# Kernel tuning notes

Measured on AMD Instinct MI355X. Metric: run time of the kernel, lower is better.

The kernel has to match this reference:

```python
import jax, jax.numpy as jnp
import numpy as np

HID, INP, BATCH, TIME = 1024, 512, 128, 256


def _kaiming(key, d1, d2, gain):
    # kaiming_normal_: std = gain / sqrt(fan_in), fan_in = d2
    return jax.random.normal(key, (d1, d2), jnp.float32) * (gain / np.sqrt(d2))


def setup_inputs() -> dict:
    key = jax.random.key(0)
    ks = jax.random.split(key, 9)
    g_lin = 1.0          # nonlinearity='linear'
    g_tanh = 5.0 / 3.0   # nonlinearity='tanh'
    inp = {
        "x": jax.random.normal(ks[0], (BATCH, TIME, INP), jnp.float32),
        "c": jnp.zeros((HID, BATCH), jnp.float32),
        "h": jnp.zeros((HID, BATCH), jnp.float32),
        "W_gx": _kaiming(ks[1], HID, INP, g_lin),
        "W_ix": _kaiming(ks[2], HID, INP, g_lin),
        "W_fx": _kaiming(ks[3], HID, INP, g_lin),
        "W_ox": _kaiming(ks[4], HID, INP, g_lin),
        "W_gh": _kaiming(ks[5], HID, HID, g_tanh),
        "W_ih": _kaiming(ks[6], HID, HID, g_tanh),
        "W_fh": _kaiming(ks[7], HID, HID, g_tanh),
        "W_oh": _kaiming(ks[8], HID, HID, g_tanh),
        "b_g": jnp.zeros((HID, 1), jnp.float32),
        "b_i": jnp.zeros((HID, 1), jnp.float32),
        "b_f": jnp.zeros((HID, 1), jnp.float32),
        "b_o": jnp.zeros((HID, 1), jnp.float32),
    }
    return inp


def reference(x, c, h, W_gx, W_ix, W_fx, W_ox, W_gh, W_ih, W_fh, W_oh,
              b_g, b_i, b_f, b_o):
    Hd = W_gx.shape[0]
    # Fuse the four gate GEMMs into one: same math, single contraction.
    Wx = jnp.concatenate([W_gx, W_ix, W_fx, W_ox], axis=0)   # (4H, I)
    Wh = jnp.concatenate([W_gh, W_ih, W_fh, W_oh], axis=0)   # (4H, H)
    b = jnp.concatenate([b_g, b_i, b_f, b_o], axis=0)[:, 0]  # (4H,)
    # Precompute all input projections: (T, B, 4H)
    xs = jnp.einsum('bti,gi->tbg', x, Wx)

    def step(carry, xt):
        c_t, h_t = carry                      # (B, H)
        z = xt + h_t @ Wh.T + b               # (B, 4H)
        g = jnp.tanh(z[:, :Hd])
        i = jax.nn.sigmoid(z[:, Hd:2 * Hd])
        f = jax.nn.sigmoid(z[:, 2 * Hd:3 * Hd])
        o = jax.nn.sigmoid(z[:, 3 * Hd:])
        c_n = g * i + c_t * f
        h_n = jnp.tanh(c_n) * o
        return (c_n, h_n), None

    (c_f, h_f), _ = jax.lax.scan(step, (c.T, h.T), xs)
    return h_f.T  # (H, B), matching the torch layout
```

## Files before the change

### kernel.cpp

```cpp
#include <hip/hip_runtime.h>
#include <cstdint>
#include <cstddef>

#define HID 1024
#define INP 512
#define BATCH 128
#define TSTEPS 256
#define NK16 96
#define HSLOTS 32
#define NBLK_CHUNK 256
#define HSLOT ((size_t)64 * 4 * 2 * 512)

using short8  = __attribute__((ext_vector_type(8))) short;
using f32x16  = __attribute__((ext_vector_type(16))) float;

#define LD8(p) (*(const short8*)(p))
#define MFMA32(a,b,c) __builtin_amdgcn_mfma_f32_32x32x16_bf16((a),(b),(c),0,0,0)

static __device__ __forceinline__ unsigned short f2bf(float f) {
    union { float f; unsigned int u; } v; v.f = f;
    unsigned int r = v.u + 0x7fffu + ((v.u >> 16) & 1u);
    return (unsigned short)(r >> 16);
}
static __device__ __forceinline__ float bf2f(unsigned short b) {
    union { unsigned int u; float f; } v; v.u = ((unsigned int)b) << 16;
    return v.f;
}
static __device__ __forceinline__ float sigmoid_f(float z) {
    return 1.0f / (1.0f + __expf(-z));
}
static __device__ __forceinline__ float tanh_f(float z) {
    return 2.0f / (1.0f + __expf(-2.0f * z)) - 1.0f;
}


__global__ void prep_w(const float* __restrict__ Wgx, const float* __restrict__ Wix,
                       const float* __restrict__ Wfx, const float* __restrict__ Wox,
                       const float* __restrict__ Wgh, const float* __restrict__ Wih,
                       const float* __restrict__ Wfh, const float* __restrict__ Woh,
                       unsigned short* __restrict__ wfrag)
{
    const int k16 = blockIdx.x;
    const int s   = blockIdx.y;
    const int tid  = threadIdx.x;
    const int lane = tid >> 2;
    const int e0   = (tid & 3) * 2;
    const int row  = s * 32 + (lane & 31);
    const int k    = k16 * 16 + (lane >> 5) * 8 + e0;
    const int j = row >> 2;
    const int g = row & 3;
    float f0, f1;
    if (k < INP) {
        const float* wx = (g == 0 ? Wgx : g == 1 ? Wix : g == 2 ? Wfx : Wox) + (size_t)j * INP;
        f0 = wx[k]; f1 = wx[k + 1];
    } else {
        const float* wh = (g == 0 ? Wgh : g == 1 ? Wih : g == 2 ? Wfh : Woh) + (size_t)j * HID;
        f0 = wh[k - INP]; f1 = wh[k - INP + 1];
    }
    ushort2 hi, lo;
    hi.x = f2bf(f0); lo.x = f2bf(f0 - bf2f(hi.x));
    hi.y = f2bf(f1); lo.y = f2bf(f1 - bf2f(hi.y));
    unsigned short* base = wfrag + ((size_t)(s * NK16 + k16) * 2) * 512 + lane * 8 + e0;
    *(ushort2*)(base)       = hi;
    *(ushort2*)(base + 512) = lo;
}

__global__ void prep_x(const float* __restrict__ x, unsigned short* __restrict__ xfrag)
{
    const int k16x = blockIdx.x;
    const int t    = blockIdx.y;
    const int tid  = threadIdx.x;
    const int cg   = tid >> 6;
    const int lane = tid & 63;
    const int col  = cg * 32 + (lane & 31);
    const int k0   = k16x * 16 + (lane >> 5) * 8;
    const float* src = x + ((size_t)col * TSTEPS + t) * INP + k0;
    const float4 v0 = *(const float4*)(src);
    const float4 v1 = *(const float4*)(src + 4);
    ushort4 h0, l0, h1, l1;
    h0.x = f2bf(v0.x); l0.x = f2bf(v0.x - bf2f(h0.x));
    h0.y = f2bf(v0.y); l0.y = f2bf(v0.y - bf2f(h0.y));
    h0.z = f2bf(v0.z); l0.z = f2bf(v0.z - bf2f(h0.z));
    h0.w = f2bf(v0.w); l0.w = f2bf(v0.w - bf2f(h0.w));
    h1.x = f2bf(v1.x); l1.x = f2bf(v1.x - bf2f(h1.x));
    h1.y = f2bf(v1.y); l1.y = f2bf(v1.y - bf2f(h1.y));
    h1.z = f2bf(v1.z); l1.z = f2bf(v1.z - bf2f(h1.z));
    h1.w = f2bf(v1.w); l1.w = f2bf(v1.w - bf2f(h1.w));
    unsigned short* base = xfrag +
        ((size_t)(((size_t)t * 32 + k16x) * 4 + cg) * 2) * 512 + lane * 8;
    *(ushort4*)(base)           = h0;
    *(ushort4*)(base + 4)       = h1;
    *(ushort4*)(base + 512)     = l0;
    *(ushort4*)(base + 512 + 4) = l1;
}

__global__ void prep_state(const float* __restrict__ cin, const float* __restrict__ hin,
                           float* __restrict__ cdst, unsigned short* __restrict__ hslot,
                           unsigned* __restrict__ flags)
{
    if (blockIdx.x == 0) flags[threadIdx.x] = 0u;
    const int idx = blockIdx.x * 256 + threadIdx.x;
    cdst[idx] = cin[idx];
    const int j = idx >> 7;
    const int b = idx & 127;
    float f = hin[idx];
    unsigned short hh = f2bf(f);
    unsigned short hl = f2bf(f - bf2f(hh));
    const int k16h = j >> 4;
    const int hlf  = (j >> 3) & 1;
    const int e    = j & 7;
    const int cg   = b >> 5;
    const int lane = 32 * hlf + (b & 31);
    unsigned short* base = hslot +
        ((size_t)((k16h * 4 + cg) * 2) * 512) + lane * 8 + e;
    base[0]   = hh;
    base[512] = hl;
}

__global__ __launch_bounds__(512, 1) void lstm_persist(
    const unsigned short* __restrict__ wfrag,
    const unsigned short* __restrict__ xfrag,
    unsigned short* __restrict__ hbuf,
    float* __restrict__ cst,
    const float* __restrict__ bg, const float* __restrict__ bi,
    const float* __restrict__ bf_, const float* __restrict__ bo,
    float* __restrict__ outf,
    unsigned* __restrict__ flags)
{
    const int tid  = threadIdx.x;
    const int wv   = tid >> 6;
    const int lane = tid & 63;
    const int l31  = lane & 31;
    const int hl   = lane >> 5;
    const int bx   = blockIdx.x;

    const int xcd     = bx & 7;
    const int ii      = bx >> 3;
    const int s       = xcd * 16 + (ii >> 1);
    const int cb      = ii & 1;
    const int colbase = cb << 6;

    const int ejl  = tid >> 6;
    const int ecl  = tid & 63;
    const int ej   = s * 8 + ejl;
    const int ecol = colbase + ecl;
    const size_t ci = (size_t)ej * BATCH + ecol;

    const float bias0 = bg[ej], bias1 = bi[ej], bias2 = bf_[ej], bias3 = bo[ej];
    float creg = cst[ci];

    const size_t bOff = (size_t)(4 * wv + 2 * cb) * 1024 + lane * 8;
    const int k16h = s >> 1;

    const unsigned short* pAx0 = wfrag + ((size_t)(s * NK16 + wv) * 2) * 512 + lane * 8;
    const unsigned short* pAh0 = wfrag + ((size_t)(s * NK16 + 32 + wv) * 2) * 512 + lane * 8;

    __shared__ float part[8][32][64];
    __shared__ unsigned long long hstage[256];
    unsigned short* hs16 = (unsigned short*)hstage;

#pragma unroll 1
    for (int t = 0; t < TSTEPS; ++t) {
        f32x16 a0A, a0B, a1A, a1B;
#pragma unroll
        for (int r = 0; r < 16; ++r) { a0A[r]=0.f; a0B[r]=0.f; a1A[r]=0.f; a1B[r]=0.f; }

        {
            const unsigned short* pA = pAx0;
            const unsigned short* pX = xfrag + (size_t)t * 131072 + bOff;
#pragma unroll
            for (int m = 0; m < 4; ++m) {
                short8 Ah  = LD8(pA);
                short8 Al  = LD8(pA + 512);
                short8 B0h = LD8(pX);
                short8 B0l = LD8(pX + 512);
                short8 B1h = LD8(pX + 1024);
                short8 B1l = LD8(pX + 1536);
                pA += 8192; pX += 32768;
                a0A = MFMA32(Ah, B0h, a0A);
                a1A = MFMA32(Ah, B1h, a1A);
                a0B = MFMA32(Ah, B0l, a0B);
                a1B = MFMA32(Ah, B1l, a1B);
                a0A = MFMA32(Al, B0h, a0A);
                a1A = MFMA32(Al, B1h, a1A);
            }
        }

        if (t > 0) {
            const unsigned target = (unsigned)t;
            int done;
            int guard = 0;
            do {
                unsigned v = target;
                if (tid < 256)
                    v = __hip_atomic_load(&flags[tid], __ATOMIC_RELAXED,
                                          __HIP_MEMORY_SCOPE_AGENT);
                done = __syncthreads_count(v >= target);
                if (done < 512) __builtin_amdgcn_s_sleep(1);
            } while (done < 512 && ++guard < (1 << 20));
            asm volatile("" ::: "memory");
            __builtin_amdgcn_sched_barrier(0);
            if ((t & 31) == 0)
                __builtin_amdgcn_fence(__ATOMIC_ACQUIRE, "agent");
        }

        {
            const unsigned short* pA = pAh0;
            const unsigned short* pH = hbuf + (size_t)((t + HSLOTS - 1) & (HSLOTS - 1)) * HSLOT + bOff;
#pragma unroll
            for (int m = 0; m < 8; ++m) {
                short8 Ah  = LD8(pA);
                short8 Al  = LD8(pA + 512);
                short8 B0h = LD8(pH);
                short8 B0l = LD8(pH + 512);
                short8 B1h = LD8(pH + 1024);
                short8 B1l = LD8(pH + 1536);
                pA += 8192; pH += 32768;
                a0A = MFMA32(Ah, B0h, a0A);
                a1A = MFMA32(Ah, B1h, a1A);
                a0B = MFMA32(Ah, B0l, a0B);
                a1B = MFMA32(Ah, B1l, a1B);
                a0A = MFMA32(Al, B0h, a0A);
                a1A = MFMA32(Al, B1h, a1A);
            }
        }

#pragma unroll
        for (int r = 0; r < 16; ++r) {
            const int lr = (r & 3) + 8 * (r >> 2) + 4 * hl;
            part[wv][lr][l31]      = a0A[r] + a0B[r];
            part[wv][lr][32 + l31] = a1A[r] + a1B[r];
        }
        __syncthreads();

        {
            const int r0 = 4 * ejl;
            float z0g = bias0, z1g = bias1, z2g = bias2, z3g = bias3;
#pragma unroll
            for (int p = 0; p < 8; ++p) {
                z0g += part[p][r0 + 0][ecl];
                z1g += part[p][r0 + 1][ecl];
                z2g += part[p][r0 + 2][ecl];
                z3g += part[p][r0 + 3][ecl];
            }
            float gg = tanh_f(z0g);
            float ig = sigmoid_f(z1g);
            float fg = sigmoid_f(z2g);
            float og = sigmoid_f(z3g);
            float cn = gg * ig + creg * fg;
            creg = cn;
            float hh = tanh_f(cn) * og;
            unsigned short hb  = f2bf(hh);
            unsigned short hlo = f2bf(hh - bf2f(hb));
            hs16[((ecl >> 5) * 2 + 0) * 256 + (ecl & 31) * 8 + ejl] = hb;
            hs16[((ecl >> 5) * 2 + 1) * 256 + (ecl & 31) * 8 + ejl] = hlo;
            if (outf && t == TSTEPS - 1) outf[ci] = hh;
        }
        __syncthreads();

        {
            unsigned short* hout = hbuf + (size_t)(t & (HSLOTS - 1)) * HSLOT;
            if (tid < 256) {
                const int r   = tid >> 6;
                const int w   = tid & 63;
                const int cgg = 2 * cb + (r >> 1);
                const int p   = r & 1;
                const size_t uo = ((size_t)((k16h * 4 + cgg) * 2 + p)) * 512
                                + 32 * (s & 1) * 8 + w * 4;
                __hip_atomic_store((unsigned long long*)(hout + uo), hstage[tid],
                                   __ATOMIC_RELAXED, __HIP_MEMORY_SCOPE_AGENT);
            }
        }
        asm volatile("s_waitcnt vmcnt(0)" ::: "memory");
        __syncthreads();
        if (tid == 0)
            __hip_atomic_store(&flags[bx], (unsigned)(t + 1),
                               __ATOMIC_RELAXED, __HIP_MEMORY_SCOPE_AGENT);
    }
    cst[ci] = creg;
}

__global__ __launch_bounds__(512, 1) void lstm_step(
    const unsigned short* __restrict__ wfrag,
    const unsigned short* __restrict__ xfrag,
    const unsigned short* __restrict__ hin,
    unsigned short* __restrict__ hout,
    float* __restrict__ cst,
    const float* __restrict__ bg, const float* __restrict__ bi,
    const float* __restrict__ bf_, const float* __restrict__ bo,
    float* __restrict__ outf, int t)
{
    const int tid  = threadIdx.x;
    const int wv   = tid >> 6;
    const int lane = tid & 63;
    const int l31  = lane & 31;
    const int hl   = lane >> 5;
    const int bx   = blockIdx.x;

    const int xcd     = bx & 7;
    const int ii      = bx >> 3;
    const int s       = xcd * 16 + (ii >> 1);
    const int cb      = ii & 1;
    const int colbase = cb << 6;

    const int ejl  = tid >> 6;
    const int ecl  = tid & 63;
    const int ej   = s * 8 + ejl;
    const int ecol = colbase + ecl;

    float add0 = bg[ej], add1 = bi[ej], add2 = bf_[ej], add3 = bo[ej];
    const size_t ci = (size_t)ej * BATCH + ecol;
    float cold = cst[ci];

    f32x16 a0A, a0B, a1A, a1B;
#pragma unroll
    for (int r = 0; r < 16; ++r) { a0A[r]=0.f; a0B[r]=0.f; a1A[r]=0.f; a1B[r]=0.f; }

    const size_t bOff = (size_t)(4 * wv + 2 * cb) * 1024 + lane * 8;

    {
        const unsigned short* pA = wfrag + ((size_t)(s * NK16 + wv) * 2) * 512 + lane * 8;
        const unsigned short* pX = xfrag + (size_t)t * 131072 + bOff;
#pragma unroll
        for (int m = 0; m < 4; ++m) {
            short8 Ah  = LD8(pA);
            short8 Al  = LD8(pA + 512);
            short8 B0h = LD8(pX);
            short8 B0l = LD8(pX + 512);
            short8 B1h = LD8(pX + 1024);
            short8 B1l = LD8(pX + 1536);
            pA += 8192; pX += 32768;
            a0A = MFMA32(Ah, B0h, a0A);
            a1A = MFMA32(Ah, B1h, a1A);
            a0B = MFMA32(Ah, B0l, a0B);
            a1B = MFMA32(Ah, B1l, a1B);
            a0A = MFMA32(Al, B0h, a0A);
            a1A = MFMA32(Al, B1h, a1A);
        }
        const unsigned short* pH = hin + bOff;
#pragma unroll
        for (int m = 0; m < 8; ++m) {
            short8 Ah  = LD8(pA);
            short8 Al  = LD8(pA + 512);
            short8 B0h = LD8(pH);
            short8 B0l = LD8(pH + 512);
            short8 B1h = LD8(pH + 1024);
            short8 B1l = LD8(pH + 1536);
            pA += 8192; pH += 32768;
            a0A = MFMA32(Ah, B0h, a0A);
            a1A = MFMA32(Ah, B1h, a1A);
            a0B = MFMA32(Ah, B0l, a0B);
            a1B = MFMA32(Ah, B1l, a1B);
            a0A = MFMA32(Al, B0h, a0A);
            a1A = MFMA32(Al, B1h, a1A);
        }
    }

    __shared__ float part[8][32][64];
#pragma unroll
    for (int r = 0; r < 16; ++r) {
        const int lr = (r & 3) + 8 * (r >> 2) + 4 * hl;
        part[wv][lr][l31]      = a0A[r] + a0B[r];
        part[wv][lr][32 + l31] = a1A[r] + a1B[r];
    }
    __syncthreads();

    {
        const int r0 = 4 * ejl;
        float z0g = add0, z1g = add1, z2g = add2, z3g = add3;
#pragma unroll
        for (int p = 0; p < 8; ++p) {
            z0g += part[p][r0 + 0][ecl];
            z1g += part[p][r0 + 1][ecl];
            z2g += part[p][r0 + 2][ecl];
            z3g += part[p][r0 + 3][ecl];
        }
        float gg = tanh_f(z0g);
        float ig = sigmoid_f(z1g);
        float fg = sigmoid_f(z2g);
        float og = sigmoid_f(z3g);
        float cn = gg * ig + cold * fg;
        cst[ci] = cn;
        float hh = tanh_f(cn) * og;
        unsigned short hb  = f2bf(hh);
        unsigned short hlo = f2bf(hh - bf2f(hb));
        const int k16h  = s >> 1;
        const int cgg   = (colbase >> 5) + (ecl >> 5);
        const int lane8 = 32 * (s & 1) + (ecl & 31);
        unsigned short* dst = hout +
            ((size_t)((k16h * 4 + cgg) * 2) * 512) + lane8 * 8 + ejl;
        dst[0]   = hb;
        dst[512] = hlo;
        if (outf) outf[ci] = hh;
    }
}

extern "C" void kernel_launch(void* const* d_in, const int* in_sizes, int n_in,
                              void* d_out, int out_size, void* d_ws, size_t ws_size,
                              hipStream_t stream)
{
    const float* x   = (const float*)d_in[0];
    const float* c0v = (const float*)d_in[1];
    const float* h0v = (const float*)d_in[2];
    const float* Wgx = (const float*)d_in[3];
    const float* Wix = (const float*)d_in[4];
    const float* Wfx = (const float*)d_in[5];
    const float* Wox = (const float*)d_in[6];
    const float* Wgh = (const float*)d_in[7];
    const float* Wih = (const float*)d_in[8];
    const float* Wfh = (const float*)d_in[9];
    const float* Woh = (const float*)d_in[10];
    const float* bg  = (const float*)d_in[11];
    const float* bi  = (const float*)d_in[12];
    const float* bf  = (const float*)d_in[13];
    const float* bo  = (const float*)d_in[14];

    unsigned short* wfrag = (unsigned short*)d_ws;
    unsigned short* xfrag = wfrag + (size_t)128 * NK16 * 2 * 512;
    unsigned short* hbuf  = xfrag + (size_t)TSTEPS * 32 * 4 * 2 * 512;
    float* cst            = (float*)(hbuf + (size_t)HSLOTS * HSLOT);
    unsigned* flags       = (unsigned*)(cst + (size_t)HID * BATCH);

    const size_t needA = (size_t)((char*)(flags + 1024) - (char*)d_ws);
    const bool useA = (ws_size >= needA);

    float* outp = (float*)d_out;

    prep_w<<<dim3(NK16, 128), dim3(256), 0, stream>>>(Wgx, Wix, Wfx, Wox,
                                                      Wgh, Wih, Wfh, Woh, wfrag);
    prep_x<<<dim3(32, TSTEPS), dim3(256), 0, stream>>>(x, xfrag);
    prep_state<<<dim3(512), dim3(256), 0, stream>>>(c0v, h0v, cst,
                                                    hbuf + (size_t)(HSLOTS - 1) * HSLOT,
                                                    flags);

    bool done = false;
    if (useA) {
        const unsigned short* a_wfrag = wfrag;
        const unsigned short* a_xfrag = xfrag;
        unsigned short* a_hbuf = hbuf;
        float* a_cst = cst;
        const float* a_bg = bg; const float* a_bi = bi;
        const float* a_bf = bf; const float* a_bo = bo;
        float* a_out = outp;
        unsigned* a_flags = flags;
        void* kargs[] = { (void*)&a_wfrag, (void*)&a_xfrag, (void*)&a_hbuf,
                          (void*)&a_cst, (void*)&a_bg, (void*)&a_bi,
                          (void*)&a_bf, (void*)&a_bo, (void*)&a_out,
                          (void*)&a_flags };
        hipError_t ce = hipLaunchCooperativeKernel(
            (const void*)lstm_persist, dim3(NBLK_CHUNK), dim3(512),
            kargs, 0, stream);
        done = (ce == hipSuccess);
    }

    if (!done) {
        unsigned short* hfA = hbuf + (size_t)(HSLOTS - 1) * HSLOT;
        unsigned short* hfB = hbuf + (size_t)(HSLOTS - 2) * HSLOT;
        for (int t = 0; t < TSTEPS; ++t) {
            const unsigned short* hin = (t & 1) ? hfB : hfA;
            unsigned short* hout      = (t & 1) ? hfA : hfB;
            lstm_step<<<dim3(256), dim3(512), 0, stream>>>(
                wfrag, xfrag, hin, hout,
                cst, bg, bi, bf, bo,
                (t == TSTEPS - 1) ? outp : nullptr, t);
        }
    }
}
```

Measured before the change: 2.297 ms.

## Cache recurrent weights in LDS, keep input weights in registers, prefetch h

Each block loads its slice of the recurrent weight fragments (128 KB) into shared memory once and keeps the input-projection weight fragments in registers, so the per-step loop no longer reloads weights from global memory. The h operand loads are software-pipelined with a 3-deep register ring. The cross-wave partial-sum reduction is restructured into three accumulation phases over a smaller shared buffer, which adds two extra barriers per step. The h output is now written with direct 16-bit atomic scatter stores instead of being staged in shared memory. Register pressure and the 128 KB LDS footprint may limit occupancy, and the narrow scattered stores may cost more than the old 64-bit coalesced ones.

Result: slower. 2.488 ms (+8.3%).

```diff
diff --git a/kernel.cpp b/kernel.cpp
--- a/kernel.cpp
+++ b/kernel.cpp
@@ -117,7 +117,7 @@
     base[512] = hl;
 }
 
-__global__ __launch_bounds__(512, 1) void lstm_persist(
+__global__ __launch_bounds__(512, 2) void lstm_persist(
     const unsigned short* __restrict__ wfrag,
     const unsigned short* __restrict__ xfrag,
     unsigned short* __restrict__ hbuf,
@@ -151,13 +151,32 @@
 
     const size_t bOff = (size_t)(4 * wv + 2 * cb) * 1024 + lane * 8;
     const int k16h = s >> 1;
-
-    const unsigned short* pAx0 = wfrag + ((size_t)(s * NK16 + wv) * 2) * 512 + lane * 8;
-    const unsigned short* pAh0 = wfrag + ((size_t)(s * NK16 + 32 + wv) * 2) * 512 + lane * 8;
-
-    __shared__ float part[8][32][64];
-    __shared__ unsigned long long hstage[256];
-    unsigned short* hs16 = (unsigned short*)hstage;
+    const int cgg   = (colbase >> 5) + (ecl >> 5);
+    const int lane8 = 32 * (s & 1) + (ecl & 31);
+    const size_t hscat = ((size_t)((k16h * 4 + cgg) * 2) * 512) + lane8 * 8 + ejl;
+
+    __shared__ unsigned short WhLds[65536];
+    __shared__ float part[3][32][64];
+
+    {
+        const unsigned short* src = wfrag + (size_t)(s * NK16 + 32) * 2 * 512;
+#pragma unroll
+        for (int c = 0; c < 16; ++c) {
+            const int cid = c * 512 + tid;
+            *(short8*)(WhLds + (size_t)cid * 8) = LD8(src + (size_t)cid * 8);
+        }
+    }
+    short8 wxh[4], wxl[4];
+    {
+        const unsigned short* pWx = wfrag + ((size_t)(s * NK16 + wv) * 2) * 512 + lane * 8;
+#pragma unroll
+        for (int m = 0; m < 4; ++m) {
+            wxh[m] = LD8(pWx);
+            wxl[m] = LD8(pWx + 512);
+            pWx += 8192;
+        }
+    }
+    __syncthreads();
 
 #pragma unroll 1
     for (int t = 0; t < TSTEPS; ++t) {
@@ -166,23 +185,24 @@
         for (int r = 0; r < 16; ++r) { a0A[r]=0.f; a0B[r]=0.f; a1A[r]=0.f; a1B[r]=0.f; }
 
         {
-            const unsigned short* pA = pAx0;
+            short8 xh0[4], xl0[4], xh1[4], xl1[4];
             const unsigned short* pX = xfrag + (size_t)t * 131072 + bOff;
 #pragma unroll
             for (int m = 0; m < 4; ++m) {
-                short8 Ah  = LD8(pA);
-                short8 Al  = LD8(pA + 512);
-                short8 B0h = LD8(pX);
-                short8 B0l = LD8(pX + 512);
-                short8 B1h = LD8(pX + 1024);
-                short8 B1l = LD8(pX + 1536);
-                pA += 8192; pX += 32768;
-                a0A = MFMA32(Ah, B0h, a0A);
-                a1A = MFMA32(Ah, B1h, a1A);
-                a0B = MFMA32(Ah, B0l, a0B);
-                a1B = MFMA32(Ah, B1l, a1B);
-                a0A = MFMA32(Al, B0h, a0A);
-                a1A = MFMA32(Al, B1h, a1A);
+                xh0[m] = LD8(pX);
+                xl0[m] = LD8(pX + 512);
+                xh1[m] = LD8(pX + 1024);
+                xl1[m] = LD8(pX + 1536);
+                pX += 32768;
+            }
+#pragma unroll
+            for (int m = 0; m < 4; ++m) {
+                a0A = MFMA32(wxh[m], xh0[m], a0A);
+                a1A = MFMA32(wxh[m], xh1[m], a1A);
+                a0B = MFMA32(wxh[m], xl0[m], a0B);
+                a1B = MFMA32(wxh[m], xl1[m], a1B);
+                a0A = MFMA32(wxl[m], xh0[m], a0A);
+                a1A = MFMA32(wxl[m], xh1[m], a1A);
             }
         }
 
@@ -205,44 +225,75 @@
         }
 
         {
-            const unsigned short* pA = pAh0;
-            const unsigned short* pH = hbuf + (size_t)((t + HSLOTS - 1) & (HSLOTS - 1)) * HSLOT + bOff;
+            const unsigned short* pH = hbuf
+                + (size_t)((t + HSLOTS - 1) & (HSLOTS - 1)) * HSLOT + bOff;
+            short8 bh0[3], bl0[3], bh1[3], bl1[3];
+#pragma unroll
+            for (int i = 0; i < 2; ++i) {
+                bh0[i] = LD8(pH);
+                bl0[i] = LD8(pH + 512);
+                bh1[i] = LD8(pH + 1024);
+                bl1[i] = LD8(pH + 1536);
+                pH += 32768;
+            }
 #pragma unroll
             for (int m = 0; m < 8; ++m) {
-                short8 Ah  = LD8(pA);
-                short8 Al  = LD8(pA + 512);
-                short8 B0h = LD8(pH);
-                short8 B0l = LD8(pH + 512);
-                short8 B1h = LD8(pH + 1024);
-                short8 B1l = LD8(pH + 1536);
-                pA += 8192; pH += 32768;
-                a0A = MFMA32(Ah, B0h, a0A);
-                a1A = MFMA32(Ah, B1h, a1A);
-                a0B = MFMA32(Ah, B0l, a0B);
-                a1B = MFMA32(Ah, B1l, a1B);
-                a0A = MFMA32(Al, B0h, a0A);
-                a1A = MFMA32(Al, B1h, a1A);
-            }
-        }
-
-#pragma unroll
-        for (int r = 0; r < 16; ++r) {
-            const int lr = (r & 3) + 8 * (r >> 2) + 4 * hl;
-            part[wv][lr][l31]      = a0A[r] + a0B[r];
-            part[wv][lr][32 + l31] = a1A[r] + a1B[r];
+                const int cur = m % 3;
+                const int nxt = (m + 2) % 3;
+                if (m < 6) {
+                    bh0[nxt] = LD8(pH);
+                    bl0[nxt] = LD8(pH + 512);
+                    bh1[nxt] = LD8(pH + 1024);
+                    bl1[nxt] = LD8(pH + 1536);
+                    pH += 32768;
+                }
+                const unsigned short* wp = WhLds + (size_t)((8 * m + wv) * 2) * 512 + lane * 8;
+                short8 Ah = *(const short8*)(wp);
+                short8 Al = *(const short8*)(wp + 512);
+                a0A = MFMA32(Ah, bh0[cur], a0A);
+                a1A = MFMA32(Ah, bh1[cur], a1A);
+                a0B = MFMA32(Ah, bl0[cur], a0B);
+                a1B = MFMA32(Ah, bl1[cur], a1B);
+                a0A = MFMA32(Al, bh0[cur], a0A);
+                a1A = MFMA32(Al, bh1[cur], a1A);
+            }
+        }
+
+        if (wv >= 5) {
+#pragma unroll
+            for (int r = 0; r < 16; ++r) {
+                const int lr = (r & 3) + 8 * (r >> 2) + 4 * hl;
+                part[wv - 5][lr][l31]      = a0A[r] + a0B[r];
+                part[wv - 5][lr][32 + l31] = a1A[r] + a1B[r];
+            }
         }
         __syncthreads();
+        if (wv >= 2 && wv < 5) {
+#pragma unroll
+            for (int r = 0; r < 16; ++r) {
+                const int lr = (r & 3) + 8 * (r >> 2) + 4 * hl;
+                part[wv - 2][lr][l31]      += a0A[r] + a0B[r];
+                part[wv - 2][lr][32 + l31] += a1A[r] + a1B[r];
+            }
+        }
+        __syncthreads();
+        if (wv < 2) {
+#pragma unroll
+            for (int r = 0; r < 16; ++r) {
+                const int lr = (r & 3) + 8 * (r >> 2) + 4 * hl;
+                part[wv][lr][l31]      += a0A[r] + a0B[r];
+                part[wv][lr][32 + l31] += a1A[r] + a1B[r];
+            }
+        }
+        __syncthreads();
 
         {
+            unsigned short* hout = hbuf + (size_t)(t & (HSLOTS - 1)) * HSLOT;
             const int r0 = 4 * ejl;
-            float z0g = bias0, z1g = bias1, z2g = bias2, z3g = bias3;
-#pragma unroll
-            for (int p = 0; p < 8; ++p) {
-                z0g += part[p][r0 + 0][ecl];
-                z1g += part[p][r0 + 1][ecl];
-                z2g += part[p][r0 + 2][ecl];
-                z3g += part[p][r0 + 3][ecl];
-            }
+            float z0g = bias0 + part[0][r0 + 0][ecl] + part[1][r0 + 0][ecl] + part[2][r0 + 0][ecl];
+            float z1g = bias1 + part[0][r0 + 1][ecl] + part[1][r0 + 1][ecl] + part[2][r0 + 1][ecl];
+            float z2g = bias2 + part[0][r0 + 2][ecl] + part[1][r0 + 2][ecl] + part[2][r0 + 2][ecl];
+            float z3g = bias3 + part[0][r0 + 3][ecl] + part[1][r0 + 3][ecl] + part[2][r0 + 3][ecl];
             float gg = tanh_f(z0g);
             float ig = sigmoid_f(z1g);
             float fg = sigmoid_f(z2g);
@@ -252,25 +303,13 @@
             float hh = tanh_f(cn) * og;
             unsigned short hb  = f2bf(hh);
             unsigned short hlo = f2bf(hh - bf2f(hb));
-            hs16[((ecl >> 5) * 2 + 0) * 256 + (ecl & 31) * 8 + ejl] = hb;
-            hs16[((ecl >> 5) * 2 + 1) * 256 + (ecl & 31) * 8 + ejl] = hlo;
+            __hip_atomic_store(hout + hscat, hb,
+                               __ATOMIC_RELAXED, __HIP_MEMORY_SCOPE_AGENT);
+            __hip_atomic_store(hout + hscat + 512, hlo,
+                               __ATOMIC_RELAXED, __HIP_MEMORY_SCOPE_AGENT);
             if (outf && t == TSTEPS - 1) outf[ci] = hh;
         }
-        __syncthreads();
-
-        {
-            unsigned short* hout = hbuf + (size_t)(t & (HSLOTS - 1)) * HSLOT;
-            if (tid < 256) {
-                const int r   = tid >> 6;
-                const int w   = tid & 63;
-                const int cgg = 2 * cb + (r >> 1);
-                const int p   = r & 1;
-                const size_t uo = ((size_t)((k16h * 4 + cgg) * 2 + p)) * 512
-                                + 32 * (s & 1) * 8 + w * 4;
-                __hip_atomic_store((unsigned long long*)(hout + uo), hstage[tid],
-                                   __ATOMIC_RELAXED, __HIP_MEMORY_SCOPE_AGENT);
-            }
-        }
+
         asm volatile("s_waitcnt vmcnt(0)" ::: "memory");
         __syncthreads();
         if (tid == 0)
```

## Split persistent LSTM into 512 batch-quartered blocks with register-resident weights

Applied to the files above, without the earlier changes.

The persistent kernel now launches 512 blocks of 256 threads. Each block owns one 8-row gate slice for one quarter of the batch (32 columns), and two blocks share a CU. Each block keeps its input-weight hi/lo fragments and its recurrent-weight hi fragments in registers across all timesteps, which removes the repeated weight loads from global memory. Synchronisation now uses four independent flag groups, so a block waits only on the 128 blocks handling the same batch quarter. The trade-off is higher register pressure, with 32 short8 arrays held per thread, and more blocks taking part in the polling.

Measured after the change: 3.006 ms. +30.9%, slower.

```diff
diff --git a/kernel.cpp b/kernel.cpp
--- a/kernel.cpp
+++ b/kernel.cpp
@@ -8,7 +8,7 @@
 #define TSTEPS 256
 #define NK16 96
 #define HSLOTS 32
-#define NBLK_CHUNK 256
+#define NBLK 512
 #define HSLOT ((size_t)64 * 4 * 2 * 512)
 
 using short8  = __attribute__((ext_vector_type(8))) short;
@@ -98,7 +98,7 @@
                            float* __restrict__ cdst, unsigned short* __restrict__ hslot,
                            unsigned* __restrict__ flags)
 {
-    if (blockIdx.x == 0) flags[threadIdx.x] = 0u;
+    if (blockIdx.x < 2) flags[blockIdx.x * 256 + threadIdx.x] = 0u;
     const int idx = blockIdx.x * 256 + threadIdx.x;
     cdst[idx] = cin[idx];
     const int j = idx >> 7;
@@ -117,7 +117,7 @@
     base[512] = hl;
 }
 
-__global__ __launch_bounds__(512, 1) void lstm_persist(
+__global__ __launch_bounds__(256, 2) void lstm_persist(
     const unsigned short* __restrict__ wfrag,
     const unsigned short* __restrict__ xfrag,
     unsigned short* __restrict__ hbuf,
@@ -134,14 +134,14 @@
     const int hl   = lane >> 5;
     const int bx   = blockIdx.x;
 
-    const int xcd     = bx & 7;
-    const int ii      = bx >> 3;
-    const int s       = xcd * 16 + (ii >> 1);
-    const int cb      = ii & 1;
-    const int colbase = cb << 6;
-
-    const int ejl  = tid >> 6;
-    const int ecl  = tid & 63;
+    const int xcd = bx & 7;
+    const int ii  = bx >> 3;
+    const int s   = xcd * 16 + (ii >> 2);
+    const int q   = ii & 3;
+    const int colbase = q << 5;
+
+    const int ejl  = tid >> 5;
+    const int ecl  = tid & 31;
     const int ej   = s * 8 + ejl;
     const int ecol = colbase + ecl;
     const size_t ci = (size_t)ej * BATCH + ecol;
@@ -149,40 +149,52 @@
     const float bias0 = bg[ej], bias1 = bi[ej], bias2 = bf_[ej], bias3 = bo[ej];
     float creg = cst[ci];
 
-    const size_t bOff = (size_t)(4 * wv + 2 * cb) * 1024 + lane * 8;
-    const int k16h = s >> 1;
-
-    const unsigned short* pAx0 = wfrag + ((size_t)(s * NK16 + wv) * 2) * 512 + lane * 8;
-    const unsigned short* pAh0 = wfrag + ((size_t)(s * NK16 + 32 + wv) * 2) * 512 + lane * 8;
-
-    __shared__ float part[8][32][64];
-    __shared__ unsigned long long hstage[256];
+    const size_t laneoff = (size_t)lane * 8;
+    const int myflag = q * 128 + s;
+    const unsigned* netflags = flags + q * 128;
+
+    __shared__ float part[4][32][32];
+    __shared__ unsigned long long hstage[128];
     unsigned short* hs16 = (unsigned short*)hstage;
+
+    short8 Wxh[8], Wxl[8], Whh[16];
+#pragma unroll
+    for (int m = 0; m < 8; ++m) {
+        const unsigned short* p = wfrag + (size_t)(s * NK16 + 4 * m + wv) * 1024 + laneoff;
+        Wxh[m] = LD8(p);
+        Wxl[m] = LD8(p + 512);
+    }
+#pragma unroll
+    for (int m = 0; m < 16; ++m) {
+        const unsigned short* p = wfrag + (size_t)(s * NK16 + 32 + 4 * m + wv) * 1024 + laneoff;
+        Whh[m] = LD8(p);
+    }
+    const unsigned short* pWhl = wfrag + (size_t)(s * NK16 + 32) * 1024 + 512 + laneoff;
 
 #pragma unroll 1
     for (int t = 0; t < TSTEPS; ++t) {
-        f32x16 a0A, a0B, a1A, a1B;
-#pragma unroll
-        for (int r = 0; r < 16; ++r) { a0A[r]=0.f; a0B[r]=0.f; a1A[r]=0.f; a1B[r]=0.f; }
+        f32x16 aA, aB;
+#pragma unroll
+        for (int r = 0; r < 16; ++r) { aA[r] = 0.f; aB[r] = 0.f; }
 
         {
-            const unsigned short* pA = pAx0;
-            const unsigned short* pX = xfrag + (size_t)t * 131072 + bOff;
-#pragma unroll
-            for (int m = 0; m < 4; ++m) {
-                short8 Ah  = LD8(pA);
-                short8 Al  = LD8(pA + 512);
-                short8 B0h = LD8(pX);
-                short8 B0l = LD8(pX + 512);
-                short8 B1h = LD8(pX + 1024);
-                short8 B1l = LD8(pX + 1536);
-                pA += 8192; pX += 32768;
-                a0A = MFMA32(Ah, B0h, a0A);
-                a1A = MFMA32(Ah, B1h, a1A);
-                a0B = MFMA32(Ah, B0l, a0B);
-                a1B = MFMA32(Ah, B1l, a1B);
-                a0A = MFMA32(Al, B0h, a0A);
-                a1A = MFMA32(Al, B1h, a1A);
+            const unsigned short* px = xfrag + (size_t)t * 131072
+                                     + (size_t)q * 1024 + laneoff;
+#pragma unroll
+            for (int g2 = 0; g2 < 2; ++g2) {
+                short8 xh[4], xl[4];
+#pragma unroll
+                for (int m = 0; m < 4; ++m) {
+                    const unsigned short* pp = px + (size_t)(4 * (4 * g2 + m) + wv) * 4096;
+                    xh[m] = LD8(pp);
+                    xl[m] = LD8(pp + 512);
+                }
+#pragma unroll
+                for (int m = 0; m < 4; ++m) {
+                    aA = MFMA32(Wxh[4 * g2 + m], xh[m], aA);
+                    aB = MFMA32(Wxh[4 * g2 + m], xl[m], aB);
+                    aA = MFMA32(Wxl[4 * g2 + m], xh[m], aA);
+                }
             }
         }
 
@@ -192,12 +204,12 @@
             int guard = 0;
             do {
                 unsigned v = target;
-                if (tid < 256)
-                    v = __hip_atomic_load(&flags[tid], __ATOMIC_RELAXED,
+                if (tid < 128)
+                    v = __hip_atomic_load(&netflags[tid], __ATOMIC_RELAXED,
                                           __HIP_MEMORY_SCOPE_AGENT);
                 done = __syncthreads_count(v >= target);
-                if (done < 512) __builtin_amdgcn_s_sleep(1);
-            } while (done < 512 && ++guard < (1 << 20));
+                if (done < 256) __builtin_amdgcn_s_sleep(1);
+            } while (done < 256 && ++guard < (1 << 20));
             asm volatile("" ::: "memory");
             __builtin_amdgcn_sched_barrier(0);
             if ((t & 31) == 0)
@@ -205,44 +217,38 @@
         }
 
         {
-            const unsigned short* pA = pAh0;
-            const unsigned short* pH = hbuf + (size_t)((t + HSLOTS - 1) & (HSLOTS - 1)) * HSLOT + bOff;
-#pragma unroll
-            for (int m = 0; m < 8; ++m) {
-                short8 Ah  = LD8(pA);
-                short8 Al  = LD8(pA + 512);
-                short8 B0h = LD8(pH);
-                short8 B0l = LD8(pH + 512);
-                short8 B1h = LD8(pH + 1024);
-                short8 B1l = LD8(pH + 1536);
-                pA += 8192; pH += 32768;
-                a0A = MFMA32(Ah, B0h, a0A);
-                a1A = MFMA32(Ah, B1h, a1A);
-                a0B = MFMA32(Ah, B0l, a0B);
-                a1B = MFMA32(Ah, B1l, a1B);
-                a0A = MFMA32(Al, B0h, a0A);
-                a1A = MFMA32(Al, B1h, a1A);
+            const unsigned short* ph = hbuf
+                + (size_t)((t + HSLOTS - 1) & (HSLOTS - 1)) * HSLOT
+                + (size_t)q * 1024 + laneoff;
+#pragma unroll
+            for (int m = 0; m < 16; ++m) {
+                const int k = 4 * m + wv;
+                short8 Bh = LD8(ph + (size_t)k * 4096);
+                short8 Bl = LD8(ph + (size_t)k * 4096 + 512);
+                short8 Al = LD8(pWhl + (size_t)k * 1024);
+                aA = MFMA32(Whh[m], Bh, aA);
+                aB = MFMA32(Whh[m], Bl, aB);
+                aA = MFMA32(Al, Bh, aA);
             }
         }
 
 #pragma unroll
         for (int r = 0; r < 16; ++r) {
             const int lr = (r & 3) + 8 * (r >> 2) + 4 * hl;
-            part[wv][lr][l31]      = a0A[r] + a0B[r];
-            part[wv][lr][32 + l31] = a1A[r] + a1B[r];
+            part[wv][lr][l31] = aA[r] + aB[r];
         }
         __syncthreads();
 
         {
             const int r0 = 4 * ejl;
-            float z0g = bias0, z1g = bias1, z2g = bias2, z3g = bias3;
-#pragma unroll
-            for (int p = 0; p < 8; ++p) {
-                z0g += part[p][r0 + 0][ecl];
-                z1g += part[p][r0 + 1][ecl];
-                z2g += part[p][r0 + 2][ecl];
-                z3g += part[p][r0 + 3][ecl];
-            }
+            float z0g = bias0 + part[0][r0 + 0][ecl] + part[1][r0 + 0][ecl]
+                             + part[2][r0 + 0][ecl] + part[3][r0 + 0][ecl];
+            float z1g = bias1 + part[0][r0 + 1][ecl] + part[1][r0 + 1][ecl]
+                             + part[2][r0 + 1][ecl] + part[3][r0 + 1][ecl];
+            float z2g = bias2 + part[0][r0 + 2][ecl] + part[1][r0 + 2][ecl]
+                             + part[2][r0 + 2][ecl] + part[3][r0 + 2][ecl];
+            float z3g = bias3 + part[0][r0 + 3][ecl] + part[1][r0 + 3][ecl]
+                             + part[2][r0 + 3][ecl] + part[3][r0 + 3][ecl];
             float gg = tanh_f(z0g);
             float ig = sigmoid_f(z1g);
             float fg = sigmoid_f(z2g);
@@ -252,29 +258,27 @@
             float hh = tanh_f(cn) * og;
             unsigned short hb  = f2bf(hh);
             unsigned short hlo = f2bf(hh - bf2f(hb));
-            hs16[((ecl >> 5) * 2 + 0) * 256 + (ecl & 31) * 8 + ejl] = hb;
-            hs16[((ecl >> 5) * 2 + 1) * 256 + (ecl & 31) * 8 + ejl] = hlo;
+            hs16[0 * 256 + ecl * 8 + ejl] = hb;
+            hs16[1 * 256 + ecl * 8 + ejl] = hlo;
             if (outf && t == TSTEPS - 1) outf[ci] = hh;
         }
         __syncthreads();
 
         {
             unsigned short* hout = hbuf + (size_t)(t & (HSLOTS - 1)) * HSLOT;
-            if (tid < 256) {
-                const int r   = tid >> 6;
-                const int w   = tid & 63;
-                const int cgg = 2 * cb + (r >> 1);
-                const int p   = r & 1;
-                const size_t uo = ((size_t)((k16h * 4 + cgg) * 2 + p)) * 512
+            if (tid < 128) {
+                const int p = tid >> 6;
+                const int w = tid & 63;
+                const size_t uo = ((size_t)(((s >> 1) * 4 + q) * 2 + p)) * 512
                                 + 32 * (s & 1) * 8 + w * 4;
-                __hip_atomic_store((unsigned long long*)(hout + uo), hstage[tid],
+                __hip_atomic_store((unsigned long long*)(hout + uo), hstage[p * 64 + w],
                                    __ATOMIC_RELAXED, __HIP_MEMORY_SCOPE_AGENT);
             }
         }
         asm volatile("s_waitcnt vmcnt(0)" ::: "memory");
         __syncthreads();
         if (tid == 0)
-            __hip_atomic_store(&flags[bx], (unsigned)(t + 1),
+            __hip_atomic_store(&flags[myflag], (unsigned)(t + 1),
                                __ATOMIC_RELAXED, __HIP_MEMORY_SCOPE_AGENT);
     }
     cst[ci] = creg;
@@ -448,7 +452,7 @@
                           (void*)&a_bf, (void*)&a_bo, (void*)&a_out,
                           (void*)&a_flags };
         hipError_t ce = hipLaunchCooperativeKernel(
-            (const void*)lstm_persist, dim3(NBLK_CHUNK), dim3(512),
+            (const void*)lstm_persist, dim3(NBLK), dim3(256),
             kargs, 0, stream);
         done = (ce == hipSuccess);
     }
```
